# Performance work log

Hardware: AMD Instinct MI355X
Metric: run time of the kernel (lower is better)

The kernel has to match this reference:

```python
import jax, jax.numpy as jnp
import numpy as np

B, T, L, D, H, S = 8, 8, 257, 1024, 16, 8
C = D // H


def _ln(x, g, b, axes):
    mu = jnp.mean(x, axes, keepdims=True)
    var = jnp.var(x, axes, keepdims=True)
    return (x - mu) * jax.lax.rsqrt(var + 1e-5) * g + b


def setup_inputs() -> dict:
    key = jax.random.key(0)
    ks = jax.random.split(key, 16)
    r = lambda i, shape, std=0.02: jax.random.normal(ks[i], shape, jnp.float32) * std
    return dict(
        x=r(0, (B, T, L, D), 1.0),
        s=r(1, (B, S, D), 1.0),
        te=r(2, (T, D), 1.0),
        patch_mask=jnp.zeros((B, T, 1, L - 1, 1), jnp.float32),
        in_proj_w=r(3, (3 * D, D)), in_proj_b=r(4, (3 * D,)),
        out_w=r(5, (D, D)), out_b=r(6, (D,)),
        ln1_g=jnp.ones(D), ln1_b=jnp.zeros(D),
        ln2_g=jnp.ones(D), ln2_b=jnp.zeros(D),
        fc_w=r(7, (4 * D, D)), fc_b=r(8, (4 * D,)),
        proj_w=r(9, (D, 4 * D)), proj_b=r(10, (D,)),
        smlp_ln_g=jnp.ones(D), smlp_ln_b=jnp.zeros(D),
        smlp_w1=r(11, (D // 8, D), 0.001), smlp_w2=r(12, (D, D // 8), 0.001),
        lnte_g=jnp.ones((T, D)), lnte_b=jnp.zeros((T, D)),
        conv_w=r(13, (D, 1, 3), 0.001), conv_b=jnp.zeros(D),
    )


def reference(x, s, te, patch_mask, in_proj_w, in_proj_b, out_w, out_b,
              ln1_g, ln1_b, ln2_g, ln2_b, fc_w, fc_b, proj_w, proj_b,
              smlp_ln_g, smlp_ln_b, smlp_w1, smlp_w2, lnte_g, lnte_b,
              conv_w, conv_b):
    scale = 1.0 / (C ** 0.5)

    def qkv(z):
        p = z @ in_proj_w.T + in_proj_b
        return jnp.split(p, 3, axis=-1)

    heads = lambda a: a.reshape(*a.shape[:-1], H, C)

    def mlp(z):
        h = z @ fc_w.T + fc_b
        h = h * jax.nn.sigmoid(1.702 * h)  # QuickGELU
        return h @ proj_w.T + proj_b

    # ---- spatial attention (per frame) ----
    xn = _ln(x, ln1_g, ln1_b, -1)
    q, k, v = [heads(a) for a in qkv(xn)]           # [B,T,L,H,C]
    aff = jnp.einsum('ntqhc,ntkhc->ntqkh', q * scale, k)
    aff = jax.nn.softmax(aff, axis=3)               # softmax over key dim (-2)
    mix = jnp.einsum('ntqlh,ntlhc->ntqhc', aff, v)
    out = mix.reshape(B, T, L, D) @ out_w.T + out_b

    # ---- syno-token branch ----
    s_mlp = (_ln(s, smlp_ln_g, smlp_ln_b, -1) @ smlp_w1.T) @ smlp_w2.T
    sn = _ln(s + s_mlp, ln1_g, ln1_b, -1)
    te_n = _ln(te, lnte_g, lnte_b, (-2, -1))        # LayerNorm over (frames, d)
    s_q, s_k, s_v = [heads(a) for a in qkv(sn)]     # [B,S,H,C]
    te_q, te_k, te_v = [a.reshape(T, 1, H, C) for a in qkv(te_n)]

    kk = k[:, :, 1:] + te_k                          # [B,T,L-1,H,C]
    vv = v[:, :, 1:] + te_v
    s_aff = jnp.einsum('nqhc,ntkhc->ntqkh', s_q * scale, kk) + patch_mask
    s_aff = jax.nn.softmax(s_aff, axis=3)
    s_mix = jnp.einsum('ntqlh,ntlhc->ntqhc', s_aff, vv)   # [B,T,S,H,C]

    # depthwise temporal conv over frames, with residual
    z = s_mix.transpose(0, 2, 3, 4, 1).reshape(B * S, D, T)   # [B*S, D, T]
    zc = jax.lax.conv_general_dilated(
        z, conv_w, window_strides=(1,), padding=[(1, 1)],
        dimension_numbers=('NCH', 'OIH', 'NCH'), feature_group_count=D)
    z = zc + conv_b[None, :, None] + z
    s_mix = z.reshape(B, S, H, C, T).transpose(0, 4, 1, 2, 3)  # [B,T,S,H,C]
    s_mix = s_mix.mean(axis=1)                                 # [B,S,H,C]
    s_out = s_mix.reshape(B, S, D) @ out_w.T + out_b

    # ---- residual + MLP ----
    x = x + out
    x = x + mlp(_ln(x, ln2_g, ln2_b, -1))
    s = s + s_out
    s = s + mlp(_ln(s, ln2_g, ln2_b, -1))
    return (x, s)
```

## Files before the change

kernel.cpp:

```cpp
#include <hip/hip_runtime.h>
#include <hip/hip_bf16.h>

#define BB 8
#define TT 8
#define LL 257
#define DD 1024
#define HH 16
#define CC 64
#define SS 8
#define NTOK (BB*TT*LL)
#define D3 (3*DD)
#define DFF (4*DD)
#define MMAIN 16384
#define MTAIL 64

typedef unsigned short u16;
typedef __attribute__((ext_vector_type(8))) short short8;
typedef __attribute__((ext_vector_type(4))) short short4v;
typedef __attribute__((ext_vector_type(4))) float f32x4;

__device__ __forceinline__ float us2f(u16 u) {
    return __uint_as_float(((unsigned int)u) << 16);
}
__device__ __forceinline__ u16 f2us(float f) {
    unsigned int u = __float_as_uint(f);
    unsigned int rb = ((u >> 16) & 1u) + 0x7fffu;
    return (u16)((u + rb) >> 16);
}

__device__ __forceinline__ void gload_lds16(const u16* g, u16* l) {
    __builtin_amdgcn_global_load_lds(
        (__attribute__((address_space(1))) void*)(void*)g,
        (__attribute__((address_space(3))) void*)(void*)l, 16, 0, 0);
}

__global__ __launch_bounds__(256)
void cvt_w(const float* __restrict__ in, u16* __restrict__ out, int n4)
{
    int i = blockIdx.x * 256 + threadIdx.x;
    if (i >= n4) return;
    float4 v = reinterpret_cast<const float4*>(in)[i];
    ushort4 o;
    o.x = f2us(v.x); o.y = f2us(v.y); o.z = f2us(v.z); o.w = f2us(v.w);
    reinterpret_cast<ushort4*>(out)[i] = o;
}

__global__ __launch_bounds__(256)
void ln_rows(const float* __restrict__ X, const float* __restrict__ R,
             const float* __restrict__ g, const float* __restrict__ bta,
             u16* __restrict__ out, int M)
{
    int row = blockIdx.x;
    if (row >= M) return;
    const float* x = X + (size_t)row * DD;
    const float* r = R ? R + (size_t)row * DD : nullptr;
    int t = threadIdx.x;
    float v[4]; float s1 = 0.f, s2 = 0.f;
#pragma unroll
    for (int i = 0; i < 4; ++i) {
        float val = x[t + 256 * i];
        if (r) val += r[t + 256 * i];
        v[i] = val; s1 += val; s2 += val * val;
    }
#pragma unroll
    for (int o = 32; o > 0; o >>= 1) { s1 += __shfl_xor(s1, o, 64); s2 += __shfl_xor(s2, o, 64); }
    __shared__ float red[10];
    int wid = t >> 6, lane = t & 63;
    if (lane == 0) { red[wid] = s1; red[4 + wid] = s2; }
    __syncthreads();
    if (t == 0) {
        float a = red[0] + red[1] + red[2] + red[3];
        float q = red[4] + red[5] + red[6] + red[7];
        float mu = a * (1.f / DD);
        float var = q * (1.f / DD) - mu * mu;
        red[8] = mu; red[9] = rsqrtf(var + 1e-5f);
    }
    __syncthreads();
    float mu = red[8], rs = red[9];
#pragma unroll
    for (int i = 0; i < 4; ++i) {
        int c = t + 256 * i;
        out[(size_t)row * DD + c] = f2us((v[i] - mu) * rs * g[c] + bta[c]);
    }
}

__global__ __launch_bounds__(256)
void ln_te(const float* __restrict__ te, const float* __restrict__ g,
           const float* __restrict__ bta, u16* __restrict__ out)
{
    const int NE = TT * DD;
    int t = threadIdx.x;
    float s1 = 0.f, s2 = 0.f;
    for (int i = t; i < NE; i += 256) { float v = te[i]; s1 += v; s2 += v * v; }
#pragma unroll
    for (int o = 32; o > 0; o >>= 1) { s1 += __shfl_xor(s1, o, 64); s2 += __shfl_xor(s2, o, 64); }
    __shared__ float red[10];
    int wid = t >> 6, lane = t & 63;
    if (lane == 0) { red[wid] = s1; red[4 + wid] = s2; }
    __syncthreads();
    if (t == 0) {
        float a = red[0] + red[1] + red[2] + red[3];
        float q = red[4] + red[5] + red[6] + red[7];
        float mu = a / (float)NE;
        float var = q / (float)NE - mu * mu;
        red[8] = mu; red[9] = rsqrtf(var + 1e-5f);
    }
    __syncthreads();
    float mu = red[8], rs = red[9];
    for (int i = t; i < NE; i += 256)
        out[i] = f2us((te[i] - mu) * rs * g[i] + bta[i]);
}

enum { EPI_BF16 = 0, EPI_GELU = 1, EPI_RES = 2, EPI_F32 = 3 };

template<int EPI>
__global__ __launch_bounds__(512)
void gemm256(const u16* __restrict__ A, const u16* __restrict__ W,
             const float* __restrict__ bias, int M, int N, int K,
             u16* __restrict__ outB, float* __restrict__ outF,
             const float* __restrict__ res)
{
    __shared__ u16 lds[2][4][8192];
    const int tid = threadIdx.x;
    const int lane = tid & 63;
    const int wid = tid >> 6;
    const int wr = wid >> 2, wc = wid & 3;

    const int gx = gridDim.x;
    const int nwg = gx * gridDim.y;
    int bid = blockIdx.y * gx + blockIdx.x;
    int qq = nwg >> 3, rr = nwg & 7;
    int xcd = bid & 7, idx = bid >> 3;
    int nb = (xcd < rr ? xcd * (qq + 1) : rr * (qq + 1) + (xcd - rr) * qq) + idx;
    const int m0 = (nb / gx) * 256, n0 = (nb % gx) * 256;

    int u0 = tid, u1 = tid + 512;
    int g0 = u0 >> 6, kb0 = (u0 >> 4) & 3, r0 = u0 & 15;
    int g1 = u1 >> 6, kb1 = (u1 >> 4) & 3, r1 = u1 & 15;
    int ar0 = m0 + g0 * 16 + r0; if (ar0 >= M) ar0 = M - 1;
    int ar1 = m0 + g1 * 16 + r1; if (ar1 >= M) ar1 = M - 1;
    int br0 = n0 + g0 * 16 + r0;
    int br1 = n0 + g1 * 16 + r1;
    const u16* pa0 = A + (size_t)ar0 * K + kb0 * 8;
    const u16* pa1 = A + (size_t)ar1 * K + kb1 * 8;
    const u16* pb0 = W + (size_t)br0 * K + kb0 * 8;
    const u16* pb1 = W + (size_t)br1 * K + kb1 * 8;

    f32x4 acc[8][4];
#pragma unroll
    for (int i = 0; i < 8; ++i)
#pragma unroll
        for (int j = 0; j < 4; ++j)
            acc[i][j] = (f32x4){0.f, 0.f, 0.f, 0.f};

    auto stageA = [&](int kt, int s, int bf) {
        int kc = kt * 64 + s * 32;
        gload_lds16(pa0 + kc, &lds[bf][s * 2][u0 * 8]);
        gload_lds16(pa1 + kc, &lds[bf][s * 2][u1 * 8]);
    };
    auto stageB = [&](int kt, int s, int bf) {
        int kc = kt * 64 + s * 32;
        gload_lds16(pb0 + kc, &lds[bf][s * 2 + 1][u0 * 8]);
        gload_lds16(pb1 + kc, &lds[bf][s * 2 + 1][u1 * 8]);
    };

    const int nk = K >> 6;
    stageA(0, 0, 0); stageB(0, 0, 0); stageA(0, 1, 0); stageB(0, 1, 0);
    asm volatile("s_waitcnt vmcnt(4)" ::: "memory");
    __builtin_amdgcn_s_barrier();
    __builtin_amdgcn_sched_barrier(0);

    short8 bq[4];
    for (int t = 0; t < nk; ++t) {
        const int bf = t & 1, bn = bf ^ 1;
        const bool st = (t + 1 < nk);
        if (st) stageA(t + 1, 0, bn);
        {
            short8 aq[4];
#pragma unroll
            for (int j = 0; j < 4; ++j)
                bq[j] = *reinterpret_cast<const short8*>(&lds[bf][1][(wc * 4 + j) * 512 + lane * 8]);
#pragma unroll
            for (int i = 0; i < 4; ++i)
                aq[i] = *reinterpret_cast<const short8*>(&lds[bf][0][(wr * 8 + i) * 512 + lane * 8]);
            __builtin_amdgcn_s_setprio(1);
#pragma unroll
            for (int i = 0; i < 4; ++i)
#pragma unroll
                for (int j = 0; j < 4; ++j)
                    acc[i][j] = __builtin_amdgcn_mfma_f32_16x16x32_bf16(aq[i], bq[j], acc[i][j], 0, 0, 0);
            __builtin_amdgcn_s_setprio(0);
        }
        __builtin_amdgcn_s_barrier();
        if (st) stageB(t + 1, 0, bn);
        {
            short8 aq[4];
#pragma unroll
            for (int i = 0; i < 4; ++i)
                aq[i] = *reinterpret_cast<const short8*>(&lds[bf][0][(wr * 8 + 4 + i) * 512 + lane * 8]);
            __builtin_amdgcn_s_setprio(1);
#pragma unroll
            for (int i = 0; i < 4; ++i)
#pragma unroll
                for (int j = 0; j < 4; ++j)
                    acc[4 + i][j] = __builtin_amdgcn_mfma_f32_16x16x32_bf16(aq[i], bq[j], acc[4 + i][j], 0, 0, 0);
            __builtin_amdgcn_s_setprio(0);
        }
        if (st) asm volatile("s_waitcnt vmcnt(4)" ::: "memory");
        else    asm volatile("s_waitcnt vmcnt(0)" ::: "memory");
        __builtin_amdgcn_s_barrier();
        __builtin_amdgcn_sched_barrier(0);
        if (st) stageA(t + 1, 1, bn);
        {
            short8 aq[4];
#pragma unroll
            for (int j = 0; j < 4; ++j)
                bq[j] = *reinterpret_cast<const short8*>(&lds[bf][3][(wc * 4 + j) * 512 + lane * 8]);
#pragma unroll
            for (int i = 0; i < 4; ++i)
                aq[i] = *reinterpret_cast<const short8*>(&lds[bf][2][(wr * 8 + i) * 512 + lane * 8]);
            __builtin_amdgcn_s_setprio(1);
#pragma unroll
            for (int i = 0; i < 4; ++i)
#pragma unroll
                for (int j = 0; j < 4; ++j)
                    acc[i][j] = __builtin_amdgcn_mfma_f32_16x16x32_bf16(aq[i], bq[j], acc[i][j], 0, 0, 0);
            __builtin_amdgcn_s_setprio(0);
        }
        __builtin_amdgcn_s_barrier();
        if (st) stageB(t + 1, 1, bn);
        {
            short8 aq[4];
#pragma unroll
            for (int i = 0; i < 4; ++i)
                aq[i] = *reinterpret_cast<const short8*>(&lds[bf][2][(wr * 8 + 4 + i) * 512 + lane * 8]);
            __builtin_amdgcn_s_setprio(1);
#pragma unroll
            for (int i = 0; i < 4; ++i)
#pragma unroll
                for (int j = 0; j < 4; ++j)
                    acc[4 + i][j] = __builtin_amdgcn_mfma_f32_16x16x32_bf16(aq[i], bq[j], acc[4 + i][j], 0, 0, 0);
            __builtin_amdgcn_s_setprio(0);
        }
        if (st) asm volatile("s_waitcnt vmcnt(4)" ::: "memory");
        __builtin_amdgcn_s_barrier();
        __builtin_amdgcn_sched_barrier(0);
    }

    const int cn = lane & 15, cr = (lane >> 4) * 4;
#pragma unroll
    for (int i = 0; i < 8; ++i) {
#pragma unroll
        for (int r = 0; r < 4; ++r) {
            int m = m0 + wr * 128 + i * 16 + cr + r;
            if (m >= M) continue;
#pragma unroll
            for (int j = 0; j < 4; ++j) {
                int n = n0 + wc * 64 + j * 16 + cn;
                float c = acc[i][j][r];
                if (bias) c += bias[n];
                size_t o = (size_t)m * N + n;
                if (EPI == EPI_BF16) outB[o] = f2us(c);
                else if (EPI == EPI_GELU) { float gg = c / (1.f + __expf(-1.702f * c)); outB[o] = f2us(gg); }
                else if (EPI == EPI_RES) outF[o] = res[o] + c;
                else outF[o] = c;
            }
        }
    }
}

template<int EPI>
__global__ __launch_bounds__(256)
void gemm_mfma(const u16* __restrict__ A, const u16* __restrict__ W,
               const float* __restrict__ bias, int M, int N, int K,
               u16* __restrict__ outB, float* __restrict__ outF,
               const float* __restrict__ res)
{
    __shared__ u16 Als[3][128 * 32];
    __shared__ u16 Bls[3][128 * 32];
    const int tid = threadIdx.x;
    const int lane = tid & 63;
    const int wid = tid >> 6;
    const int wm = (wid >> 1) * 64, wn = (wid & 1) * 64;

    const int gx = gridDim.x;
    const int nwg = gx * gridDim.y;
    int bid = blockIdx.y * gx + blockIdx.x;
    int qq = nwg >> 3, rr = nwg & 7;
    int xcd = bid & 7, idx = bid >> 3;
    int nb = (xcd < rr ? xcd * (qq + 1) : rr * (qq + 1) + (xcd - rr) * qq) + idx;
    const int m0 = (nb / gx) * 128, n0 = (nb % gx) * 128;

    int o0 = tid, o1 = tid + 256;
    int g0 = o0 >> 6, kb0 = (o0 >> 4) & 3, r0 = o0 & 15;
    int g1 = o1 >> 6, kb1 = (o1 >> 4) & 3, r1 = o1 & 15;
    int ar0 = m0 + g0 * 16 + r0; if (ar0 >= M) ar0 = M - 1;
    int ar1 = m0 + g1 * 16 + r1; if (ar1 >= M) ar1 = M - 1;
    int br0 = n0 + g0 * 16 + r0;
    int br1 = n0 + g1 * 16 + r1;
    const u16* a0 = A + (size_t)ar0 * K + kb0 * 8;
    const u16* a1 = A + (size_t)ar1 * K + kb1 * 8;
    const u16* b0 = W + (size_t)br0 * K + kb0 * 8;
    const u16* b1 = W + (size_t)br1 * K + kb1 * 8;

    f32x4 acc[4][4];
#pragma unroll
    for (int i = 0; i < 4; ++i)
#pragma unroll
        for (int j = 0; j < 4; ++j)
            acc[i][j] = (f32x4){0.f, 0.f, 0.f, 0.f};

    auto stage = [&](int kt, int sl) {
        int kk = kt << 5;
        gload_lds16(a0 + kk, &Als[sl][o0 * 8]);
        gload_lds16(a1 + kk, &Als[sl][o1 * 8]);
        gload_lds16(b0 + kk, &Bls[sl][o0 * 8]);
        gload_lds16(b1 + kk, &Bls[sl][o1 * 8]);
    };
    auto compute = [&](int sl) {
        short8 af[4], bfr[4];
#pragma unroll
        for (int i = 0; i < 4; ++i)
            af[i] = *reinterpret_cast<const short8*>(&Als[sl][((wm >> 4) + i) * 512 + lane * 8]);
#pragma unroll
        for (int j = 0; j < 4; ++j)
            bfr[j] = *reinterpret_cast<const short8*>(&Bls[sl][((wn >> 4) + j) * 512 + lane * 8]);
        __builtin_amdgcn_s_setprio(1);
#pragma unroll
        for (int i = 0; i < 4; ++i)
#pragma unroll
            for (int j = 0; j < 4; ++j)
                acc[i][j] = __builtin_amdgcn_mfma_f32_16x16x32_bf16(af[i], bfr[j], acc[i][j], 0, 0, 0);
        __builtin_amdgcn_s_setprio(0);
    };

    const int nk = K >> 5;
    stage(0, 0);
    stage(1, 1);
    asm volatile("s_waitcnt vmcnt(4)" ::: "memory");
    __builtin_amdgcn_s_barrier();
    __builtin_amdgcn_sched_barrier(0);

    int t = 0;
    for (; t < nk - 2; ++t) {
        stage(t + 2, (t + 2) % 3);
        compute(t % 3);
        asm volatile("s_waitcnt vmcnt(4)" ::: "memory");
        __builtin_amdgcn_s_barrier();
        __builtin_amdgcn_sched_barrier(0);
    }
    compute(t % 3);
    asm volatile("s_waitcnt vmcnt(0)" ::: "memory");
    __builtin_amdgcn_s_barrier();
    __builtin_amdgcn_sched_barrier(0);
    ++t;
    compute(t % 3);

    const int cn = lane & 15, cr = (lane >> 4) * 4;
#pragma unroll
    for (int i = 0; i < 4; ++i) {
#pragma unroll
        for (int r = 0; r < 4; ++r) {
            int m = m0 + wm + i * 16 + cr + r;
            if (m >= M) continue;
#pragma unroll
            for (int j = 0; j < 4; ++j) {
                int n = n0 + wn + j * 16 + cn;
                float c = acc[i][j][r];
                if (bias) c += bias[n];
                size_t o = (size_t)m * N + n;
                if (EPI == EPI_BF16) outB[o] = f2us(c);
                else if (EPI == EPI_GELU) { float gg = c / (1.f + __expf(-1.702f * c)); outB[o] = f2us(gg); }
                else if (EPI == EPI_RES) outF[o] = res[o] + c;
                else outF[o] = c;
            }
        }
    }
}

#define KSTR 72
#define VSTR 296
#define PSTR 40

__global__ __launch_bounds__(256)
void spatial_attn(const u16* __restrict__ qkv, u16* __restrict__ mix)
{
    const int h = blockIdx.x, bt = blockIdx.y;
    const int hoff = h * CC;
    const size_t base = (size_t)bt * LL * D3;
    __shared__ u16 Kls[257 * KSTR];
    __shared__ u16 Vt[64 * VSTR];
    __shared__ u16 Pb[4][16 * PSTR];
    const int tid = threadIdx.x, lane = tid & 63, w = tid >> 6;
    const int c15 = lane & 15, g = lane >> 4;

    for (int idx = tid; idx < 257 * 8; idx += 256) {
        int row = idx >> 3, c8 = (idx & 7) << 3;
        float4 v = *reinterpret_cast<const float4*>(&qkv[base + (size_t)row * D3 + DD + hoff + c8]);
        *reinterpret_cast<float4*>(&Kls[row * KSTR + c8]) = v;
    }
    for (int idx = tid; idx < 288 * 64; idx += 256) {
        int key = idx >> 6, c = idx & 63;
        u16 v = 0;
        if (key < 257) v = qkv[base + (size_t)key * D3 + 2 * DD + hoff + c];
        Vt[c * VSTR + key] = v;
    }
    __syncthreads();

    u16* pb = Pb[w];
    for (int qt = w; qt < 17; qt += 4) {
        int qrow = qt * 16 + c15; if (qrow > 256) qrow = 256;
        const u16* qp = &qkv[base + (size_t)qrow * D3 + hoff + g * 8];
        short8 a0 = *reinterpret_cast<const short8*>(qp);
        short8 a1 = *reinterpret_cast<const short8*>(qp + 32);

        f32x4 sc[17];
#pragma unroll
        for (int t = 0; t < 17; ++t) sc[t] = (f32x4){0.f, 0.f, 0.f, 0.f};
        __builtin_amdgcn_s_setprio(1);
#pragma unroll
        for (int t = 0; t < 17; ++t) {
            int krow = t * 16 + c15; if (krow > 256) krow = 256;
            short8 b0 = *reinterpret_cast<const short8*>(&Kls[krow * KSTR + g * 8]);
            short8 b1 = *reinterpret_cast<const short8*>(&Kls[krow * KSTR + 32 + g * 8]);
            sc[t] = __builtin_amdgcn_mfma_f32_16x16x32_bf16(a0, b0, sc[t], 0, 0, 0);
            sc[t] = __builtin_amdgcn_mfma_f32_16x16x32_bf16(a1, b1, sc[t], 0, 0, 0);
        }
        __builtin_amdgcn_s_setprio(0);

        const bool lastv = (c15 == 0);
#pragma unroll
        for (int r = 0; r < 4; ++r) {
            float mx = -1e30f;
#pragma unroll
            for (int t = 0; t < 17; ++t) {
                float v = sc[t][r] * 0.125f;
                if (t == 16 && !lastv) v = -1e30f;
                sc[t][r] = v;
                mx = fmaxf(mx, v);
            }
            mx = fmaxf(mx, __shfl_xor(mx, 1, 64));
            mx = fmaxf(mx, __shfl_xor(mx, 2, 64));
            mx = fmaxf(mx, __shfl_xor(mx, 4, 64));
            mx = fmaxf(mx, __shfl_xor(mx, 8, 64));
            float sum = 0.f;
#pragma unroll
            for (int t = 0; t < 17; ++t) { float e = __expf(sc[t][r] - mx); sc[t][r] = e; sum += e; }
            sum += __shfl_xor(sum, 1, 64);
            sum += __shfl_xor(sum, 2, 64);
            sum += __shfl_xor(sum, 4, 64);
            sum += __shfl_xor(sum, 8, 64);
            float is = 1.f / sum;
#pragma unroll
            for (int t = 0; t < 17; ++t) sc[t][r] *= is;
        }

        f32x4 oacc[4];
#pragma unroll
        for (int ct = 0; ct < 4; ++ct) oacc[ct] = (f32x4){0.f, 0.f, 0.f, 0.f};
#pragma unroll
        for (int k0 = 0; k0 < 9; ++k0) {
            const int t0 = 2 * k0, t1 = 2 * k0 + 1;
#pragma unroll
            for (int r = 0; r < 4; ++r) {
                pb[(4 * g + r) * PSTR + c15]      = f2us(sc[t0][r]);
                pb[(4 * g + r) * PSTR + 16 + c15] = (t1 < 17) ? f2us(sc[t1][r]) : (u16)0;
            }
            short8 pa = *reinterpret_cast<const short8*>(&pb[c15 * PSTR + 8 * g]);
            __builtin_amdgcn_s_setprio(1);
#pragma unroll
            for (int ct = 0; ct < 4; ++ct) {
                short8 vb = *reinterpret_cast<const short8*>(&Vt[(16 * ct + c15) * VSTR + 32 * k0 + 8 * g]);
                oacc[ct] = __builtin_amdgcn_mfma_f32_16x16x32_bf16(pa, vb, oacc[ct], 0, 0, 0);
            }
            __builtin_amdgcn_s_setprio(0);
        }

#pragma unroll
        for (int r = 0; r < 4; ++r) {
            int q = qt * 16 + 4 * g + r;
            if (q >= LL) continue;
            size_t ob = ((size_t)bt * LL + q) * DD + hoff;
#pragma unroll
            for (int ct = 0; ct < 4; ++ct)
                mix[ob + 16 * ct + c15] = f2us(oacc[ct][r]);
        }
    }
}

#define SK 68

__global__ __launch_bounds__(256)
void s_attn(const u16* __restrict__ qkv, const u16* __restrict__ snqkv,
            const u16* __restrict__ teqkv, const float* __restrict__ pmask,
            float* __restrict__ smix)
{
    const int h = blockIdx.x, bt = blockIdx.y, b = bt >> 3, t = bt & 7;
    const int hoff = h * CC;
    const int tid = threadIdx.x, lane = tid & 63, w = tid >> 6;
    __shared__ u16 Kls[256 * SK];
    __shared__ u16 Vls[256 * SK];
    __shared__ float pls[4][256];
    const size_t base = (size_t)bt * LL * D3;

    const int c8 = (tid & 7) * 8;
    const u16* tekp = &teqkv[t * D3 + DD + hoff + c8];
    const u16* tevp = &teqkv[t * D3 + 2 * DD + hoff + c8];
    float tek[8], tev[8];
#pragma unroll
    for (int j = 0; j < 8; ++j) { tek[j] = us2f(tekp[j]); tev[j] = us2f(tevp[j]); }
#pragma unroll
    for (int pass = 0; pass < 8; ++pass) {
        int key = (tid >> 3) + 32 * pass;
        const u16* kp = &qkv[base + (size_t)(key + 1) * D3 + DD + hoff + c8];
        const u16* vp = &qkv[base + (size_t)(key + 1) * D3 + 2 * DD + hoff + c8];
        short4v k0 = *reinterpret_cast<const short4v*>(kp);
        short4v k1 = *reinterpret_cast<const short4v*>(kp + 4);
        short4v v0 = *reinterpret_cast<const short4v*>(vp);
        short4v v1 = *reinterpret_cast<const short4v*>(vp + 4);
        short4v ok0, ok1, ov0, ov1;
#pragma unroll
        for (int j = 0; j < 4; ++j) {
            ok0[j] = (short)f2us(us2f((u16)k0[j]) + tek[j]);
            ok1[j] = (short)f2us(us2f((u16)k1[j]) + tek[4 + j]);
            ov0[j] = (short)f2us(us2f((u16)v0[j]) + tev[j]);
            ov1[j] = (short)f2us(us2f((u16)v1[j]) + tev[4 + j]);
        }
        *reinterpret_cast<short4v*>(&Kls[key * SK + c8]) = ok0;
        *reinterpret_cast<short4v*>(&Kls[key * SK + c8 + 4]) = ok1;
        *reinterpret_cast<short4v*>(&Vls[key * SK + c8]) = ov0;
        *reinterpret_cast<short4v*>(&Vls[key * SK + c8 + 4]) = ov1;
    }
    __syncthreads();

    const float* pm = pmask + (size_t)bt * 256;
    for (int qi = w; qi < SS; qi += 4) {
        float qc = us2f(snqkv[(size_t)(b * SS + qi) * D3 + hoff + lane]) * 0.125f;
        float sc[4] = {0.f, 0.f, 0.f, 0.f};
        for (int c = 0; c < CC; ++c) {
            float qv = __shfl(qc, c, 64);
#pragma unroll
            for (int j = 0; j < 4; ++j)
                sc[j] += qv * us2f(Kls[(lane + 64 * j) * SK + c]);
        }
#pragma unroll
        for (int j = 0; j < 4; ++j) sc[j] += pm[lane + 64 * j];
        float mx = fmaxf(fmaxf(sc[0], sc[1]), fmaxf(sc[2], sc[3]));
#pragma unroll
        for (int o = 32; o > 0; o >>= 1) mx = fmaxf(mx, __shfl_xor(mx, o, 64));
        float sum = 0.f;
#pragma unroll
        for (int j = 0; j < 4; ++j) { sc[j] = __expf(sc[j] - mx); sum += sc[j]; }
#pragma unroll
        for (int o = 32; o > 0; o >>= 1) sum += __shfl_xor(sum, o, 64);
        float inv = 1.f / sum;
#pragma unroll
        for (int j = 0; j < 4; ++j) pls[w][lane + 64 * j] = sc[j] * inv;
        float acc = 0.f;
        for (int key = 0; key < 256; ++key)
            acc += pls[w][key] * us2f(Vls[key * SK + lane]);
        smix[(((size_t)bt * SS + qi) * HH + h) * CC + lane] = acc;
    }
}

__global__ __launch_bounds__(256)
void conv_mean(const float* __restrict__ smix, const float* __restrict__ cw,
               const float* __restrict__ cb, u16* __restrict__ out)
{
    int idx = blockIdx.x * 256 + threadIdx.x;
    int d = idx & 1023;
    int bs = idx >> 10;
    int b = bs >> 3, s_ = bs & 7;
    float z[TT];
#pragma unroll
    for (int t = 0; t < TT; ++t)
        z[t] = smix[((size_t)(b * TT + t) * SS + s_) * DD + d];
    float w0 = cw[d * 3], w1 = cw[d * 3 + 1], w2 = cw[d * 3 + 2];
    float acc = 0.f;
#pragma unroll
    for (int t = 0; t < TT; ++t) {
        float zc = w1 * z[t];
        if (t > 0)      zc += w0 * z[t - 1];
        if (t < TT - 1) zc += w2 * z[t + 1];
        acc += z[t] + zc;
    }
    out[(size_t)bs * DD + d] = f2us(acc * 0.125f + cb[d]);
}

extern "C" void kernel_launch(void* const* d_in, const int* in_sizes, int n_in,
                              void* d_out, int out_size, void* d_ws, size_t ws_size,
                              hipStream_t stream)
{
    const float* x      = (const float*)d_in[0];
    const float* s      = (const float*)d_in[1];
    const float* te     = (const float*)d_in[2];
    const float* pmask  = (const float*)d_in[3];
    const float* in_w   = (const float*)d_in[4];
    const float* in_b   = (const float*)d_in[5];
    const float* out_w  = (const float*)d_in[6];
    const float* out_b  = (const float*)d_in[7];
    const float* ln1_g  = (const float*)d_in[8];
    const float* ln1_b  = (const float*)d_in[9];
    const float* ln2_g  = (const float*)d_in[10];
    const float* ln2_b  = (const float*)d_in[11];
    const float* fc_w   = (const float*)d_in[12];
    const float* fc_b   = (const float*)d_in[13];
    const float* proj_w = (const float*)d_in[14];
    const float* proj_b = (const float*)d_in[15];
    const float* smlp_g = (const float*)d_in[16];
    const float* smlp_b = (const float*)d_in[17];
    const float* w1     = (const float*)d_in[18];
    const float* w2     = (const float*)d_in[19];
    const float* lnte_g = (const float*)d_in[20];
    const float* lnte_b = (const float*)d_in[21];
    const float* conv_w = (const float*)d_in[22];
    const float* conv_b = (const float*)d_in[23];

    float* outx = (float*)d_out;
    float* outs = outx + (size_t)NTOK * DD;

    char* ws = (char*)d_ws;
    u16* qkv    = (u16*)ws;
    u16* mixb   = (u16*)(ws + (size_t)NTOK * D3 * 2);
    u16* hidden = qkv;
    u16* xn     = (u16*)(ws + (size_t)NTOK * DFF * 2);
    char* sm    = ws + (size_t)NTOK * DFF * 2 + (size_t)NTOK * DD * 2;
    u16*  s_ln0 = (u16*)sm;   sm += 64 * DD * 2;
    u16*  h1    = (u16*)sm;   sm += 64 * 128 * 2;
    float* smlp = (float*)sm; sm += 64 * DD * 4;
    u16*  sn    = (u16*)sm;   sm += 64 * DD * 2;
    u16*  snqkv = (u16*)sm;   sm += 64 * D3 * 2;
    u16*  ten   = (u16*)sm;   sm += 8 * DD * 2;
    u16*  teqkv = (u16*)sm;   sm += 8 * D3 * 2;
    float* smix = (float*)sm; sm += (size_t)BB * TT * SS * DD * 4;
    u16*  smm   = (u16*)sm;   sm += 64 * DD * 2;
    u16*  ln2s  = (u16*)sm;   sm += 64 * DD * 2;
    u16*  hids  = (u16*)sm;   sm += 64 * DFF * 2;
    u16* in_wb   = (u16*)sm;  sm += (size_t)D3 * DD * 2;
    u16* out_wb  = (u16*)sm;  sm += (size_t)DD * DD * 2;
    u16* fc_wb   = (u16*)sm;  sm += (size_t)DFF * DD * 2;
    u16* proj_wb = (u16*)sm;  sm += (size_t)DD * DFF * 2;
    u16* w1b     = (u16*)sm;  sm += (size_t)128 * DD * 2;
    u16* w2b     = (u16*)sm;  sm += (size_t)DD * 128 * 2;

    const float* FNULL = nullptr;
    u16* UNULL = nullptr;

    auto cvt = [&](const float* src, u16* dst, int n) {
        hipLaunchKernelGGL(cvt_w, dim3((n / 4 + 255) / 256), dim3(256), 0, stream, src, dst, n / 4);
    };
    cvt(in_w,   in_wb,   D3 * DD);
    cvt(out_w,  out_wb,  DD * DD);
    cvt(fc_w,   fc_wb,   DFF * DD);
    cvt(proj_w, proj_wb, DD * DFF);
    cvt(w1,     w1b,     128 * DD);
    cvt(w2,     w2b,     DD * 128);

    const int MT64 = MMAIN / 256;

    hipLaunchKernelGGL(ln_rows, dim3(NTOK), dim3(256), 0, stream, x, FNULL, ln1_g, ln1_b, xn, NTOK);
    hipLaunchKernelGGL((gemm256<EPI_BF16>), dim3(D3 / 256, MT64), dim3(512), 0, stream,
                       xn, in_wb, in_b, MMAIN, D3, DD, qkv, (float*)nullptr, FNULL);
    hipLaunchKernelGGL((gemm_mfma<EPI_BF16>), dim3(D3 / 128, 1), dim3(256), 0, stream,
                       xn + (size_t)MMAIN * DD, in_wb, in_b, MTAIL, D3, DD,
                       qkv + (size_t)MMAIN * D3, (float*)nullptr, FNULL);
    hipLaunchKernelGGL(spatial_attn, dim3(HH, BB * TT), dim3(256), 0, stream, qkv, mixb);
    hipLaunchKernelGGL((gemm256<EPI_RES>), dim3(DD / 256, MT64), dim3(512), 0, stream,
                       mixb, out_wb, out_b, MMAIN, DD, DD, UNULL, outx, x);
    hipLaunchKernelGGL((gemm_mfma<EPI_RES>), dim3(DD / 128, 1), dim3(256), 0, stream,
                       mixb + (size_t)MMAIN * DD, out_wb, out_b, MTAIL, DD, DD,
                       UNULL, outx + (size_t)MMAIN * DD, x + (size_t)MMAIN * DD);
    hipLaunchKernelGGL(ln_rows, dim3(64), dim3(256), 0, stream, s, FNULL, smlp_g, smlp_b, s_ln0, 64);
    hipLaunchKernelGGL((gemm_mfma<EPI_BF16>), dim3(1, 1), dim3(256), 0, stream,
                       s_ln0, w1b, FNULL, 64, 128, DD, h1, (float*)nullptr, FNULL);
    hipLaunchKernelGGL((gemm_mfma<EPI_F32>), dim3(DD / 128, 1), dim3(256), 0, stream,
                       h1, w2b, FNULL, 64, DD, 128, UNULL, smlp, FNULL);
    hipLaunchKernelGGL(ln_rows, dim3(64), dim3(256), 0, stream, s, smlp, ln1_g, ln1_b, sn, 64);
    hipLaunchKernelGGL(ln_te, dim3(1), dim3(256), 0, stream, te, lnte_g, lnte_b, ten);
    hipLaunchKernelGGL((gemm_mfma<EPI_BF16>), dim3(D3 / 128, 1), dim3(256), 0, stream,
                       sn, in_wb, in_b, 64, D3, DD, snqkv, (float*)nullptr, FNULL);
    hipLaunchKernelGGL((gemm_mfma<EPI_BF16>), dim3(D3 / 128, 1), dim3(256), 0, stream,
                       ten, in_wb, in_b, 8, D3, DD, teqkv, (float*)nullptr, FNULL);
    hipLaunchKernelGGL(s_attn, dim3(HH, BB * TT), dim3(256), 0, stream, qkv, snqkv, teqkv, pmask, smix);
    hipLaunchKernelGGL(conv_mean, dim3(256), dim3(256), 0, stream, smix, conv_w, conv_b, smm);
    hipLaunchKernelGGL((gemm_mfma<EPI_RES>), dim3(DD / 128, 1), dim3(256), 0, stream,
                       smm, out_wb, out_b, 64, DD, DD, UNULL, outs, s);
    hipLaunchKernelGGL(ln_rows, dim3(NTOK), dim3(256), 0, stream, outx, FNULL, ln2_g, ln2_b, xn, NTOK);
    hipLaunchKernelGGL((gemm256<EPI_GELU>), dim3(DFF / 256, MT64), dim3(512), 0, stream,
                       xn, fc_wb, fc_b, MMAIN, DFF, DD, hidden, (float*)nullptr, FNULL);
    hipLaunchKernelGGL((gemm_mfma<EPI_GELU>), dim3(DFF / 128, 1), dim3(256), 0, stream,
                       xn + (size_t)MMAIN * DD, fc_wb, fc_b, MTAIL, DFF, DD,
                       hidden + (size_t)MMAIN * DFF, (float*)nullptr, FNULL);
    hipLaunchKernelGGL((gemm256<EPI_RES>), dim3(DD / 256, MT64), dim3(512), 0, stream,
                       hidden, proj_wb, proj_b, MMAIN, DD, DFF, UNULL, outx, outx);
    hipLaunchKernelGGL((gemm_mfma<EPI_RES>), dim3(DD / 128, 1), dim3(256), 0, stream,
                       hidden + (size_t)MMAIN * DFF, proj_wb, proj_b, MTAIL, DD, DFF,
                       UNULL, outx + (size_t)MMAIN * DD, outx + (size_t)MMAIN * DD);
    hipLaunchKernelGGL(ln_rows, dim3(64), dim3(256), 0, stream, outs, FNULL, ln2_g, ln2_b, ln2s, 64);
    hipLaunchKernelGGL((gemm_mfma<EPI_GELU>), dim3(DFF / 128, 1), dim3(256), 0, stream,
                       ln2s, fc_wb, fc_b, 64, DFF, DD, hids, (float*)nullptr, FNULL);
    hipLaunchKernelGGL((gemm_mfma<EPI_RES>), dim3(DD / 128, 1), dim3(256), 0, stream,
                       hids, proj_wb, proj_b, 64, DD, DFF, UNULL, outs, outs);
}
```

Before: 1.488 ms.

## Fuse syno-token prep into one kernel and restructure GEMM LDS read/barrier schedule

Merges the small syno-token chain (LN, two tiny MLP matmuls, second LN, and the frame-embedding LN) into a single 65-block kernel. The sn and te_n rows now share one 72-row QKV GEMM instead of two launches, which removes about six small kernel launches and their intermediate buffers. Separately, the main 256x256 GEMM loop now issues its LDS fragment reads before the global prefetch and adds barriers around each MFMA phase, changing how loads overlap with compute. The small MLP now runs on scalar FMA instead of MFMA, and the extra barriers could add stalls in the dominant GEMMs.

```diff
diff --git a/kernel.cpp b/kernel.cpp
--- a/kernel.cpp
+++ b/kernel.cpp
@@ -85,30 +85,120 @@
 }
 
 __global__ __launch_bounds__(256)
-void ln_te(const float* __restrict__ te, const float* __restrict__ g,
-           const float* __restrict__ bta, u16* __restrict__ out)
-{
-    const int NE = TT * DD;
-    int t = threadIdx.x;
-    float s1 = 0.f, s2 = 0.f;
-    for (int i = t; i < NE; i += 256) { float v = te[i]; s1 += v; s2 += v * v; }
+void s_prep(const float* __restrict__ s, const float* __restrict__ te,
+            const float* __restrict__ smlp_g, const float* __restrict__ smlp_b,
+            const float* __restrict__ ln1_g, const float* __restrict__ ln1_b,
+            const float* __restrict__ lnte_g, const float* __restrict__ lnte_b,
+            const u16* __restrict__ w1b, const u16* __restrict__ w2b,
+            u16* __restrict__ snte)
+{
+    const int blk = blockIdx.x, t = threadIdx.x;
+    __shared__ float red[10];
+    const int wid = t >> 6, lane = t & 63;
+
+    if (blk == 64) {
+        const int NE = TT * DD;
+        float s1 = 0.f, s2 = 0.f;
+        for (int i = t; i < NE; i += 256) { float v = te[i]; s1 += v; s2 += v * v; }
+#pragma unroll
+        for (int o = 32; o > 0; o >>= 1) { s1 += __shfl_xor(s1, o, 64); s2 += __shfl_xor(s2, o, 64); }
+        if (lane == 0) { red[wid] = s1; red[4 + wid] = s2; }
+        __syncthreads();
+        if (t == 0) {
+            float a = red[0] + red[1] + red[2] + red[3];
+            float q = red[4] + red[5] + red[6] + red[7];
+            float mu = a / (float)NE;
+            float var = q / (float)NE - mu * mu;
+            red[8] = mu; red[9] = rsqrtf(var + 1e-5f);
+        }
+        __syncthreads();
+        float mu = red[8], rs = red[9];
+        for (int i = t; i < NE; i += 256)
+            snte[(size_t)64 * DD + i] = f2us((te[i] - mu) * rs * lnte_g[i] + lnte_b[i]);
+        return;
+    }
+
+    __shared__ float xrow[1024];
+    __shared__ float h1[128];
+    const float* sr = s + (size_t)blk * DD;
+
+    float v[4]; float s1 = 0.f, s2 = 0.f;
+#pragma unroll
+    for (int i = 0; i < 4; ++i) {
+        float val = sr[t + 256 * i];
+        v[i] = val; s1 += val; s2 += val * val;
+    }
 #pragma unroll
     for (int o = 32; o > 0; o >>= 1) { s1 += __shfl_xor(s1, o, 64); s2 += __shfl_xor(s2, o, 64); }
-    __shared__ float red[10];
-    int wid = t >> 6, lane = t & 63;
     if (lane == 0) { red[wid] = s1; red[4 + wid] = s2; }
     __syncthreads();
     if (t == 0) {
         float a = red[0] + red[1] + red[2] + red[3];
         float q = red[4] + red[5] + red[6] + red[7];
-        float mu = a / (float)NE;
-        float var = q / (float)NE - mu * mu;
+        float mu = a * (1.f / DD);
+        float var = q * (1.f / DD) - mu * mu;
         red[8] = mu; red[9] = rsqrtf(var + 1e-5f);
     }
     __syncthreads();
-    float mu = red[8], rs = red[9];
-    for (int i = t; i < NE; i += 256)
-        out[i] = f2us((te[i] - mu) * rs * g[i] + bta[i]);
+    {
+        float mu = red[8], rs = red[9];
+#pragma unroll
+        for (int i = 0; i < 4; ++i) {
+            int c = t + 256 * i;
+            xrow[c] = (v[i] - mu) * rs * smlp_g[c] + smlp_b[c];
+        }
+    }
+    __syncthreads();
+    if (t < 128) {
+        const u16* wr_ = w1b + (size_t)t * DD;
+        float a0 = 0.f, a1 = 0.f;
+        for (int k = 0; k < DD; k += 8) {
+            short4v wa = *reinterpret_cast<const short4v*>(&wr_[k]);
+            short4v wb = *reinterpret_cast<const short4v*>(&wr_[k + 4]);
+#pragma unroll
+            for (int j = 0; j < 4; ++j) {
+                a0 += xrow[k + j] * us2f((u16)wa[j]);
+                a1 += xrow[k + 4 + j] * us2f((u16)wb[j]);
+            }
+        }
+        h1[t] = a0 + a1;
+    }
+    __syncthreads();
+    float w[4]; s1 = 0.f; s2 = 0.f;
+#pragma unroll
+    for (int i = 0; i < 4; ++i) {
+        int d = t + 256 * i;
+        const u16* w2r = w2b + (size_t)d * 128;
+        float a = 0.f;
+        for (int k = 0; k < 128; k += 4) {
+            short4v wa = *reinterpret_cast<const short4v*>(&w2r[k]);
+#pragma unroll
+            for (int j = 0; j < 4; ++j) a += h1[k + j] * us2f((u16)wa[j]);
+        }
+        float val = sr[d] + a;
+        w[i] = val; s1 += val; s2 += val * val;
+    }
+#pragma unroll
+    for (int o = 32; o > 0; o >>= 1) { s1 += __shfl_xor(s1, o, 64); s2 += __shfl_xor(s2, o, 64); }
+    __syncthreads();
+    if (lane == 0) { red[wid] = s1; red[4 + wid] = s2; }
+    __syncthreads();
+    if (t == 0) {
+        float a = red[0] + red[1] + red[2] + red[3];
+        float q = red[4] + red[5] + red[6] + red[7];
+        float mu = a * (1.f / DD);
+        float var = q * (1.f / DD) - mu * mu;
+        red[8] = mu; red[9] = rsqrtf(var + 1e-5f);
+    }
+    __syncthreads();
+    {
+        float mu = red[8], rs = red[9];
+#pragma unroll
+        for (int i = 0; i < 4; ++i) {
+            int d = t + 256 * i;
+            snte[(size_t)blk * DD + d] = f2us((w[i] - mu) * rs * ln1_g[d] + ln1_b[d]);
+        }
+    }
 }
 
 enum { EPI_BF16 = 0, EPI_GELU = 1, EPI_RES = 2, EPI_F32 = 3 };
@@ -170,78 +260,72 @@
     __builtin_amdgcn_s_barrier();
     __builtin_amdgcn_sched_barrier(0);
 
-    short8 bq[4];
     for (int t = 0; t < nk; ++t) {
         const int bf = t & 1, bn = bf ^ 1;
         const bool st = (t + 1 < nk);
+        short8 aq[4], bq[4];
+#pragma unroll
+        for (int j = 0; j < 4; ++j)
+            bq[j] = *reinterpret_cast<const short8*>(&lds[bf][1][(wc * 4 + j) * 512 + lane * 8]);
+#pragma unroll
+        for (int i = 0; i < 4; ++i)
+            aq[i] = *reinterpret_cast<const short8*>(&lds[bf][0][(wr * 8 + i) * 512 + lane * 8]);
         if (st) stageA(t + 1, 0, bn);
-        {
-            short8 aq[4];
+        __builtin_amdgcn_s_barrier();
+        __builtin_amdgcn_s_setprio(1);
+#pragma unroll
+        for (int i = 0; i < 4; ++i)
 #pragma unroll
             for (int j = 0; j < 4; ++j)
-                bq[j] = *reinterpret_cast<const short8*>(&lds[bf][1][(wc * 4 + j) * 512 + lane * 8]);
-#pragma unroll
-            for (int i = 0; i < 4; ++i)
-                aq[i] = *reinterpret_cast<const short8*>(&lds[bf][0][(wr * 8 + i) * 512 + lane * 8]);
-            __builtin_amdgcn_s_setprio(1);
-#pragma unroll
-            for (int i = 0; i < 4; ++i)
-#pragma unroll
-                for (int j = 0; j < 4; ++j)
-                    acc[i][j] = __builtin_amdgcn_mfma_f32_16x16x32_bf16(aq[i], bq[j], acc[i][j], 0, 0, 0);
-            __builtin_amdgcn_s_setprio(0);
-        }
-        __builtin_amdgcn_s_barrier();
+                acc[i][j] = __builtin_amdgcn_mfma_f32_16x16x32_bf16(aq[i], bq[j], acc[i][j], 0, 0, 0);
+        __builtin_amdgcn_s_setprio(0);
+        __builtin_amdgcn_s_barrier();
+        __builtin_amdgcn_sched_barrier(0);
+#pragma unroll
+        for (int i = 0; i < 4; ++i)
+            aq[i] = *reinterpret_cast<const short8*>(&lds[bf][0][(wr * 8 + 4 + i) * 512 + lane * 8]);
         if (st) stageB(t + 1, 0, bn);
-        {
-            short8 aq[4];
-#pragma unroll
-            for (int i = 0; i < 4; ++i)
-                aq[i] = *reinterpret_cast<const short8*>(&lds[bf][0][(wr * 8 + 4 + i) * 512 + lane * 8]);
-            __builtin_amdgcn_s_setprio(1);
-#pragma unroll
-            for (int i = 0; i < 4; ++i)
-#pragma unroll
-                for (int j = 0; j < 4; ++j)
-                    acc[4 + i][j] = __builtin_amdgcn_mfma_f32_16x16x32_bf16(aq[i], bq[j], acc[4 + i][j], 0, 0, 0);
-            __builtin_amdgcn_s_setprio(0);
-        }
+        __builtin_amdgcn_s_barrier();
+        __builtin_amdgcn_s_setprio(1);
+#pragma unroll
+        for (int i = 0; i < 4; ++i)
+#pragma unroll
+            for (int j = 0; j < 4; ++j)
+                acc[4 + i][j] = __builtin_amdgcn_mfma_f32_16x16x32_bf16(aq[i], bq[j], acc[4 + i][j], 0, 0, 0);
+        __builtin_amdgcn_s_setprio(0);
         if (st) asm volatile("s_waitcnt vmcnt(4)" ::: "memory");
         else    asm volatile("s_waitcnt vmcnt(0)" ::: "memory");
         __builtin_amdgcn_s_barrier();
         __builtin_amdgcn_sched_barrier(0);
+#pragma unroll
+        for (int j = 0; j < 4; ++j)
+            bq[j] = *reinterpret_cast<const short8*>(&lds[bf][3][(wc * 4 + j) * 512 + lane * 8]);
+#pragma unroll
+        for (int i = 0; i < 4; ++i)
+            aq[i] = *reinterpret_cast<const short8*>(&lds[bf][2][(wr * 8 + i) * 512 + lane * 8]);
         if (st) stageA(t + 1, 1, bn);
-        {
-            short8 aq[4];
+        __builtin_amdgcn_s_barrier();
+        __builtin_amdgcn_s_setprio(1);
+#pragma unroll
+        for (int i = 0; i < 4; ++i)
 #pragma unroll
             for (int j = 0; j < 4; ++j)
-                bq[j] = *reinterpret_cast<const short8*>(&lds[bf][3][(wc * 4 + j) * 512 + lane * 8]);
-#pragma unroll
-            for (int i = 0; i < 4; ++i)
-                aq[i] = *reinterpret_cast<const short8*>(&lds[bf][2][(wr * 8 + i) * 512 + lane * 8]);
-            __builtin_amdgcn_s_setprio(1);
-#pragma unroll
-            for (int i = 0; i < 4; ++i)
-#pragma unroll
-                for (int j = 0; j < 4; ++j)
-                    acc[i][j] = __builtin_amdgcn_mfma_f32_16x16x32_bf16(aq[i], bq[j], acc[i][j], 0, 0, 0);
-            __builtin_amdgcn_s_setprio(0);
-        }
-        __builtin_amdgcn_s_barrier();
+                acc[i][j] = __builtin_amdgcn_mfma_f32_16x16x32_bf16(aq[i], bq[j], acc[i][j], 0, 0, 0);
+        __builtin_amdgcn_s_setprio(0);
+        __builtin_amdgcn_s_barrier();
+        __builtin_amdgcn_sched_barrier(0);
+#pragma unroll
+        for (int i = 0; i < 4; ++i)
+            aq[i] = *reinterpret_cast<const short8*>(&lds[bf][2][(wr * 8 + 4 + i) * 512 + lane * 8]);
         if (st) stageB(t + 1, 1, bn);
-        {
-            short8 aq[4];
-#pragma unroll
-            for (int i = 0; i < 4; ++i)
-                aq[i] = *reinterpret_cast<const short8*>(&lds[bf][2][(wr * 8 + 4 + i) * 512 + lane * 8]);
-            __builtin_amdgcn_s_setprio(1);
-#pragma unroll
-            for (int i = 0; i < 4; ++i)
-#pragma unroll
-                for (int j = 0; j < 4; ++j)
-                    acc[4 + i][j] = __builtin_amdgcn_mfma_f32_16x16x32_bf16(aq[i], bq[j], acc[4 + i][j], 0, 0, 0);
-            __builtin_amdgcn_s_setprio(0);
-        }
+        __builtin_amdgcn_s_barrier();
+        __builtin_amdgcn_s_setprio(1);
+#pragma unroll
+        for (int i = 0; i < 4; ++i)
+#pragma unroll
+            for (int j = 0; j < 4; ++j)
+                acc[4 + i][j] = __builtin_amdgcn_mfma_f32_16x16x32_bf16(aq[i], bq[j], acc[4 + i][j], 0, 0, 0);
+        __builtin_amdgcn_s_setprio(0);
         if (st) asm volatile("s_waitcnt vmcnt(4)" ::: "memory");
         __builtin_amdgcn_s_barrier();
         __builtin_amdgcn_sched_barrier(0);
@@ -625,13 +709,8 @@
     u16* hidden = qkv;
     u16* xn     = (u16*)(ws + (size_t)NTOK * DFF * 2);
     char* sm    = ws + (size_t)NTOK * DFF * 2 + (size_t)NTOK * DD * 2;
-    u16*  s_ln0 = (u16*)sm;   sm += 64 * DD * 2;
-    u16*  h1    = (u16*)sm;   sm += 64 * 128 * 2;
-    float* smlp = (float*)sm; sm += 64 * DD * 4;
-    u16*  sn    = (u16*)sm;   sm += 64 * DD * 2;
-    u16*  snqkv = (u16*)sm;   sm += 64 * D3 * 2;
-    u16*  ten   = (u16*)sm;   sm += 8 * DD * 2;
-    u16*  teqkv = (u16*)sm;   sm += 8 * D3 * 2;
+    u16*  snte   = (u16*)sm;  sm += (size_t)72 * DD * 2;
+    u16*  sqkv72 = (u16*)sm;  sm += (size_t)72 * D3 * 2;
     float* smix = (float*)sm; sm += (size_t)BB * TT * SS * DD * 4;
     u16*  smm   = (u16*)sm;   sm += 64 * DD * 2;
     u16*  ln2s  = (u16*)sm;   sm += 64 * DD * 2;
@@ -670,18 +749,12 @@
     hipLaunchKernelGGL((gemm_mfma<EPI_RES>), dim3(DD / 128, 1), dim3(256), 0, stream,
                        mixb + (size_t)MMAIN * DD, out_wb, out_b, MTAIL, DD, DD,
                        UNULL, outx + (size_t)MMAIN * DD, x + (size_t)MMAIN * DD);
-    hipLaunchKernelGGL(ln_rows, dim3(64), dim3(256), 0, stream, s, FNULL, smlp_g, smlp_b, s_ln0, 64);
-    hipLaunchKernelGGL((gemm_mfma<EPI_BF16>), dim3(1, 1), dim3(256), 0, stream,
-                       s_ln0, w1b, FNULL, 64, 128, DD, h1, (float*)nullptr, FNULL);
-    hipLaunchKernelGGL((gemm_mfma<EPI_F32>), dim3(DD / 128, 1), dim3(256), 0, stream,
-                       h1, w2b, FNULL, 64, DD, 128, UNULL, smlp, FNULL);
-    hipLaunchKernelGGL(ln_rows, dim3(64), dim3(256), 0, stream, s, smlp, ln1_g, ln1_b, sn, 64);
-    hipLaunchKernelGGL(ln_te, dim3(1), dim3(256), 0, stream, te, lnte_g, lnte_b, ten);
+    hipLaunchKernelGGL(s_prep, dim3(65), dim3(256), 0, stream,
+                       s, te, smlp_g, smlp_b, ln1_g, ln1_b, lnte_g, lnte_b, w1b, w2b, snte);
     hipLaunchKernelGGL((gemm_mfma<EPI_BF16>), dim3(D3 / 128, 1), dim3(256), 0, stream,
-                       sn, in_wb, in_b, 64, D3, DD, snqkv, (float*)nullptr, FNULL);
-    hipLaunchKernelGGL((gemm_mfma<EPI_BF16>), dim3(D3 / 128, 1), dim3(256), 0, stream,
-                       ten, in_wb, in_b, 8, D3, DD, teqkv, (float*)nullptr, FNULL);
-    hipLaunchKernelGGL(s_attn, dim3(HH, BB * TT), dim3(256), 0, stream, qkv, snqkv, teqkv, pmask, smix);
+                       snte, in_wb, in_b, 72, D3, DD, sqkv72, (float*)nullptr, FNULL);
+    hipLaunchKernelGGL(s_attn, dim3(HH, BB * TT), dim3(256), 0, stream,
+                       qkv, sqkv72, sqkv72 + (size_t)64 * D3, pmask, smix);
     hipLaunchKernelGGL(conv_mean, dim3(256), dim3(256), 0, stream, smix, conv_w, conv_b, smm);
     hipLaunchKernelGGL((gemm_mfma<EPI_RES>), dim3(DD / 128, 1), dim3(256), 0, stream,
                        smm, out_wb, out_b, 64, DD, DD, UNULL, outs, s);
```

Result: faster. 1.426 ms (-4.2%).
